# Kernel tuning notes

Hardware: AMD Instinct MI355X
Metric: run time of the kernel (lower is better)

Reference implementation:

```python
import jax, jax.numpy as jnp
import numpy as np

B, S, D_MODEL, H = 2, 2048, 2048, 16
DQK = D_MODEL // H            # 128
DV = D_MODEL * 2 // H // 3    # 85 (GLU branch)
SCALE = DQK ** -0.5
ROPE_BASE = 10000.0


def apply_rope(x):
    # x: [B, S, H, D], NeoX-style half rotation
    D = x.shape[-1]
    half = D // 2
    inv_freq = 1.0 / (ROPE_BASE ** (jnp.arange(half, dtype=jnp.float32) / half))
    ang = jnp.arange(x.shape[1], dtype=jnp.float32)[:, None] * inv_freq[None, :]  # [S, half]
    cos = jnp.cos(ang)[None, :, None, :]
    sin = jnp.sin(ang)[None, :, None, :]
    x1, x2 = x[..., :half], x[..., half:]
    return jnp.concatenate([x1 * cos - x2 * sin, x2 * cos + x1 * sin], axis=-1)


def setup_inputs() -> dict:
    key = jax.random.key(0)
    ks = jax.random.split(key, 12)
    init = lambda k, shape, fan_in: jax.random.uniform(k, shape, jnp.float32, -1.0, 1.0) * (fan_in ** -0.5)
    q = jax.random.normal(ks[0], (B, S, D_MODEL), jnp.float32)
    k = jax.random.normal(ks[1], (B, S, D_MODEL), jnp.float32)
    v = jax.random.normal(ks[2], (B, S, D_MODEL), jnp.float32)
    # causal boolean mask: True = masked (upper triangle)
    mask = jnp.triu(jnp.ones((S, S), dtype=bool), k=1)
    Wq = init(ks[3], (D_MODEL, DQK * H), D_MODEL)
    bq = init(ks[4], (DQK * H,), D_MODEL)
    Wk = init(ks[5], (D_MODEL, DQK * H), D_MODEL)
    bk = init(ks[6], (DQK * H,), D_MODEL)
    Wv = init(ks[7], (D_MODEL, DV * H * 2), D_MODEL)
    bv = init(ks[8], (DV * H * 2,), D_MODEL)
    Wo = init(ks[9], (DV * H, D_MODEL), DV * H)
    bo = init(ks[10], (D_MODEL,), DV * H)
    return {"q": q, "k": k, "v": v, "mask": mask,
            "Wq": Wq, "bq": bq, "Wk": Wk, "bk": bk,
            "Wv": Wv, "bv": bv, "Wo": Wo, "bo": bo}


def reference(q, k, v, mask, Wq, bq, Wk, bk, Wv, bv, Wo, bo):
    qp = q @ Wq + bq                      # [B,S,H*DQK]
    kp = k @ Wk + bk                      # [B,S,H*DQK]
    vp = v @ Wv + bv                      # [B,S,2*H*DV]
    # GLU over the FULL last dim (matches torch chunk(2, dim=-1) before unflatten)
    half = DV * H
    vg = vp[..., :half] * jax.nn.silu(vp[..., half:])   # [B,S,H*DV]
    qh = qp.reshape(B, S, H, DQK)
    kh = kp.reshape(B, S, H, DQK)
    vh = vg.reshape(B, S, H, DV)
    qh = apply_rope(qh)
    kh = apply_rope(kh)
    # [B,H,S,D]
    qh = qh.transpose(0, 2, 1, 3)
    kh = kh.transpose(0, 2, 1, 3)
    vh = vh.transpose(0, 2, 1, 3)
    score = jnp.einsum('bhqd,bhkd->bhqk', qh, kh) * SCALE  # [B,H,S,S]
    score = jnp.where(mask[None, None, :, :], -jnp.inf, score)
    attn = jax.nn.softmax(score, axis=-1)
    o = jnp.einsum('bhqk,bhkd->bhqd', attn, vh)            # [B,H,S,DV]
    o = o.transpose(0, 2, 1, 3).reshape(B, S, H * DV)
    return o @ Wo + bo                                     # [B,S,D_MODEL]
```

## Files before the change

kernel.cpp:

```cpp
#include <hip/hip_runtime.h>
#include <cstdint>
#include <cmath>

typedef __bf16 bf16;
typedef __bf16 bf16x8 __attribute__((ext_vector_type(8)));
typedef float f32x4 __attribute__((ext_vector_type(4)));

#define B_      2
#define S_      2048
#define H_      16
#define DQK_    128
#define DV_     85
#define DVP_    96
#define DMODEL_ 2048
#define NKV_    1360
#define KH_     1536
#define NV_     2720
#define NVP_    2816
#define SCALE_  0.08838834764831845f
#define QSCALE_ 0.12752044442215615f
#define M2_     16.0f
#define L2_10K_ 13.287712379549449f

__device__ __forceinline__ void lds_cp16(const void* g, void* l) {
    __builtin_amdgcn_global_load_lds(
        (const __attribute__((address_space(1))) unsigned int*)(uintptr_t)g,
        (__attribute__((address_space(3))) unsigned int*)(uintptr_t)l,
        16, 0, 0);
}

__global__ __launch_bounds__(256) void detect_dtype(const unsigned int* __restrict__ w,
                                                    int* __restrict__ flag) {
    __shared__ int cnt;
    if (threadIdx.x == 0) cnt = 0;
    __syncthreads();
    unsigned v = w[threadIdx.x];
    unsigned e = (v >> 7) & 0xFFu;
    if (e > 100u && e < 140u) atomicAdd(&cnt, 1);
    __syncthreads();
    if (threadIdx.x == 0) *flag = (cnt >= 200) ? 1 : 0;
}

__global__ __launch_bounds__(256) void norm_mat(const void* __restrict__ src, bf16* __restrict__ dst,
                                                const int* __restrict__ flag, long n8) {
    long i = (long)blockIdx.x * 256 + threadIdx.x;
    if (i >= n8) return;
    if (*flag) {
        ((bf16x8*)dst)[i] = ((const bf16x8*)src)[i];
    } else {
        const float* s = (const float*)src;
        bf16x8 v;
#pragma unroll
        for (int j = 0; j < 8; ++j) v[j] = (bf16)s[i * 8 + j];
        ((bf16x8*)dst)[i] = v;
    }
}

__global__ __launch_bounds__(256) void norm_bias4(
    const void* __restrict__ s0, const void* __restrict__ s1,
    const void* __restrict__ s2, const void* __restrict__ s3,
    float* __restrict__ d0, float* __restrict__ d1,
    float* __restrict__ d2, float* __restrict__ d3,
    const int* __restrict__ flag) {
    int j = blockIdx.x * 256 + threadIdx.x;
    const void* s; float* d;
    if (j < DMODEL_) { s = s0; d = d0; }
    else if ((j -= DMODEL_) < DMODEL_) { s = s1; d = d1; }
    else if ((j -= DMODEL_) < NV_) { s = s2; d = d2; }
    else if ((j -= NV_) < DMODEL_) { s = s3; d = d3; }
    else return;
    d[j] = (*flag) ? (float)((const bf16*)s)[j] : ((const float*)s)[j];
}

__global__ __launch_bounds__(256) void transpose_pad_dyn(
    const void* __restrict__ in, bf16* __restrict__ out, const int* __restrict__ flag,
    int R, int C, int Rp, int Cp) {
    __shared__ bf16 tile[32][33];
    const bool isbf = (*flag != 0);
    int r0 = blockIdx.x * 32, c0 = blockIdx.y * 32;
    int tx = threadIdx.x, ty = threadIdx.y;
#pragma unroll
    for (int i = 0; i < 32; i += 8) {
        int r = r0 + ty + i, c = c0 + tx;
        bf16 v = (bf16)0.0f;
        if (r < R && c < C) {
            size_t idx = (size_t)r * C + c;
            v = isbf ? ((const bf16*)in)[idx] : (bf16)((const float*)in)[idx];
        }
        tile[ty + i][tx] = v;
    }
    __syncthreads();
#pragma unroll
    for (int i = 0; i < 32; i += 8) {
        int oc = c0 + ty + i, orr = r0 + tx;
        if (oc < Cp && orr < Rp) out[(size_t)oc * Rp + orr] = tile[tx][ty + i];
    }
}

__global__ __launch_bounds__(256) void transpose_wo_dyn(
    const void* __restrict__ in, bf16* __restrict__ out, const int* __restrict__ flag) {
    __shared__ bf16 tile[32][33];
    const bool isbf = (*flag != 0);
    int k0 = blockIdx.x * 32, n0 = blockIdx.y * 32;
    int tx = threadIdx.x, ty = threadIdx.y;
#pragma unroll
    for (int i = 0; i < 32; i += 8) {
        int k = k0 + ty + i, c = n0 + tx;
        int hh = k / DVP_, dd = k - hh * DVP_;
        bf16 v = (bf16)0.0f;
        if (dd < DV_) {
            size_t idx = (size_t)(hh * DV_ + dd) * DMODEL_ + c;
            v = isbf ? ((const bf16*)in)[idx] : (bf16)((const float*)in)[idx];
        }
        tile[ty + i][tx] = v;
    }
    __syncthreads();
#pragma unroll
    for (int i = 0; i < 32; i += 8) {
        int n = n0 + ty + i, k = k0 + tx;
        out[(size_t)n * KH_ + k] = tile[tx][ty + i];
    }
}

__global__ __launch_bounds__(256) void gemm_qk_rope(
    const bf16* __restrict__ Aq, const bf16* __restrict__ Ak,
    const bf16* __restrict__ Btq, const bf16* __restrict__ Btk,
    const float* __restrict__ bq, const float* __restrict__ bk,
    bf16* __restrict__ qt, bf16* __restrict__ ktp) {
    __shared__ bf16 As[128 * 32];
    __shared__ bf16 Bs[128 * 32];
    __shared__ bf16 ep[64 * 132];
    const int z = blockIdx.z;
    const bf16* A    = z ? Ak  : Aq;
    const bf16* Bt   = z ? Btk : Btq;
    const float* bias = z ? bk : bq;
    bf16* dst        = z ? ktp : qt;
    const float qs   = z ? 1.0f : QSCALE_;
    const int t = threadIdx.x, lane = t & 63, w = t >> 6;
    const int m0 = blockIdx.x * 128, n0 = blockIdx.y * 128;
    const int wm = (w >> 1) * 64, wn = (w & 1) * 64;
    const int fm = lane & 15, quad = lane >> 4, fk = quad * 8;
    const int srow = lane >> 2, scol = (lane & 3) * 8;
    f32x4 acc[4][4] = {};
    for (int k0 = 0; k0 < DMODEL_; k0 += 32) {
        __syncthreads();
#pragma unroll
        for (int j = 0; j < 2; ++j) {
            int c = j * 4 + w;
            lds_cp16(A + (size_t)(m0 + c * 16 + srow) * DMODEL_ + k0 + scol, &As[c * 512]);
            lds_cp16(Bt + (size_t)(n0 + c * 16 + srow) * DMODEL_ + k0 + scol, &Bs[c * 512]);
        }
        __syncthreads();
        bf16x8 af[4], bfr[4];
#pragma unroll
        for (int i = 0; i < 4; ++i) {
            af[i]  = *(const bf16x8*)&As[(wm + i * 16 + fm) * 32 + fk];
            bfr[i] = *(const bf16x8*)&Bs[(wn + i * 16 + fm) * 32 + fk];
        }
#pragma unroll
        for (int i = 0; i < 4; ++i)
#pragma unroll
            for (int jn = 0; jn < 4; ++jn)
                acc[i][jn] = __builtin_amdgcn_mfma_f32_16x16x32_bf16(af[i], bfr[jn], acc[i][jn], 0, 0, 0);
    }
    const int h = blockIdx.y;
    const int b = m0 >> 11, s_base = m0 & (S_ - 1);
    float bv[4];
#pragma unroll
    for (int jn = 0; jn < 4; ++jn) bv[jn] = bias[n0 + wn + jn * 16 + fm];
    bf16* dbase = dst + (size_t)(b * H_ + h) * S_ * DQK_;
#pragma unroll
    for (int ph = 0; ph < 2; ++ph) {
        if ((w >> 1) == ph) {
#pragma unroll
            for (int i = 0; i < 4; ++i)
#pragma unroll
                for (int jn = 0; jn < 4; ++jn)
#pragma unroll
                    for (int r = 0; r < 4; ++r)
                        ep[(i * 16 + quad * 4 + r) * 132 + wn + jn * 16 + fm] =
                            (bf16)(acc[i][jn][r] + bv[jn]);
        }
        __syncthreads();
#pragma unroll
        for (int it2 = 0; it2 < 4; ++it2) {
            int task = it2 * 256 + t;
            int lr = task >> 4, ch = task & 15;
            int s = s_base + ph * 64 + lr;
            bf16x8 v = *(const bf16x8*)&ep[lr * 132 + ch * 8];
            bf16x8 u = *(const bf16x8*)&ep[lr * 132 + ((ch * 8) ^ 64)];
            bf16x8 o8;
#pragma unroll
            for (int j = 0; j < 8; ++j) {
                int d = ch * 8 + j, dd = d & 63;
                float ang = (float)s * exp2f(-(float)dd * (L2_10K_ / 64.0f));
                float sn, cs;
                __sincosf(ang, &sn, &cs);
                float x = (float)v[j], y = (float)u[j];
                float ov = (d < 64) ? (x * cs - y * sn) : (x * cs + y * sn);
                o8[j] = (bf16)(ov * qs);
            }
            *(bf16x8*)&dbase[(size_t)s * DQK_ + ch * 8] = o8;
        }
        __syncthreads();
    }
}

__global__ __launch_bounds__(256) void gemm_bt(
    const bf16* __restrict__ A, const bf16* __restrict__ Bt,
    const float* __restrict__ bias, bf16* __restrict__ C,
    int M, int N, int K, int Nreal, int ldc) {
    __shared__ bf16 As[128 * 32];
    __shared__ bf16 Bs[128 * 32];
    const int t = threadIdx.x, lane = t & 63, w = t >> 6;
    const int m0 = blockIdx.x * 128, n0 = blockIdx.y * 128;
    const int wm = (w >> 1) * 64, wn = (w & 1) * 64;
    const int fm = lane & 15, quad = lane >> 4, fk = quad * 8;
    const int srow = lane >> 2, scol = (lane & 3) * 8;
    f32x4 acc[4][4] = {};
    for (int k0 = 0; k0 < K; k0 += 32) {
        __syncthreads();
#pragma unroll
        for (int j = 0; j < 2; ++j) {
            int c = j * 4 + w;
            lds_cp16(A + (size_t)(m0 + c * 16 + srow) * K + k0 + scol, &As[c * 512]);
            lds_cp16(Bt + (size_t)(n0 + c * 16 + srow) * K + k0 + scol, &Bs[c * 512]);
        }
        __syncthreads();
        bf16x8 af[4], bfr[4];
#pragma unroll
        for (int i = 0; i < 4; ++i) {
            af[i]  = *(const bf16x8*)&As[(wm + i * 16 + fm) * 32 + fk];
            bfr[i] = *(const bf16x8*)&Bs[(wn + i * 16 + fm) * 32 + fk];
        }
#pragma unroll
        for (int i = 0; i < 4; ++i)
#pragma unroll
            for (int jn = 0; jn < 4; ++jn)
                acc[i][jn] = __builtin_amdgcn_mfma_f32_16x16x32_bf16(af[i], bfr[jn], acc[i][jn], 0, 0, 0);
    }
#pragma unroll
    for (int jn = 0; jn < 4; ++jn) {
        int col = n0 + wn + jn * 16 + fm;
        if (col >= Nreal) continue;
        float bv = bias[col];
#pragma unroll
        for (int i = 0; i < 4; ++i) {
            int rowb = m0 + wm + i * 16 + quad * 4;
#pragma unroll
            for (int r = 0; r < 4; ++r)
                C[(size_t)(rowb + r) * ldc + col] = (bf16)(acc[i][jn][r] + bv);
        }
    }
}

__global__ __launch_bounds__(256) void gemm_bt_oh(
    const bf16* __restrict__ Oh, const bf16* __restrict__ Bt,
    const float* __restrict__ bias, bf16* __restrict__ C, float* __restrict__ Cf,
    const int* __restrict__ outflag) {
    __shared__ bf16 As[128 * 32];
    __shared__ bf16 Bs[128 * 32];
    const int t = threadIdx.x, lane = t & 63, w = t >> 6;
    const int m0 = blockIdx.x * 128, n0 = blockIdx.y * 128;
    const int wm = (w >> 1) * 64, wn = (w & 1) * 64;
    const int fm = lane & 15, quad = lane >> 4, fk = quad * 8;
    const int srow = lane >> 2, scol = (lane & 3) * 8;
    f32x4 acc[4][4] = {};
    for (int k0 = 0; k0 < KH_; k0 += 32) {
        __syncthreads();
#pragma unroll
        for (int j = 0; j < 2; ++j) {
            int c = j * 4 + w;
            int m = m0 + c * 16 + srow;
            int k = k0 + scol;
            int hh = k / DVP_, dd = k - hh * DVP_;
            const bf16* ga = Oh + ((size_t)((m >> 11) * H_ + hh) * S_ + (m & (S_ - 1))) * DVP_ + dd;
            lds_cp16(ga, &As[c * 512]);
            lds_cp16(Bt + (size_t)(n0 + c * 16 + srow) * KH_ + k0 + scol, &Bs[c * 512]);
        }
        __syncthreads();
        bf16x8 af[4], bfr[4];
#pragma unroll
        for (int i = 0; i < 4; ++i) {
            af[i]  = *(const bf16x8*)&As[(wm + i * 16 + fm) * 32 + fk];
            bfr[i] = *(const bf16x8*)&Bs[(wn + i * 16 + fm) * 32 + fk];
        }
#pragma unroll
        for (int i = 0; i < 4; ++i)
#pragma unroll
            for (int jn = 0; jn < 4; ++jn)
                acc[i][jn] = __builtin_amdgcn_mfma_f32_16x16x32_bf16(af[i], bfr[jn], acc[i][jn], 0, 0, 0);
    }
    bool bf16out = (*outflag != 0);
#pragma unroll
    for (int jn = 0; jn < 4; ++jn) {
        int col = n0 + wn + jn * 16 + fm;
        float bv = bias[col];
#pragma unroll
        for (int i = 0; i < 4; ++i) {
            int rowb = m0 + wm + i * 16 + quad * 4;
            if (bf16out) {
#pragma unroll
                for (int r = 0; r < 4; ++r)
                    C[(size_t)(rowb + r) * DMODEL_ + col] = (bf16)(acc[i][jn][r] + bv);
            } else {
#pragma unroll
                for (int r = 0; r < 4; ++r)
                    Cf[(size_t)(rowb + r) * DMODEL_ + col] = acc[i][jn][r] + bv;
            }
        }
    }
}

__global__ __launch_bounds__(256) void swiglu_tr2(const bf16* __restrict__ vp, bf16* __restrict__ vt) {
    __shared__ bf16 tile[32][33];
    const int bh = blockIdx.x, b = bh >> 4, h = bh & 15;
    const int s0 = blockIdx.y * 32, d0 = blockIdx.z * 32;
    const int tx = threadIdx.x, ty = threadIdx.y;
#pragma unroll
    for (int i = 0; i < 32; i += 8) {
        int s = s0 + ty + i, d = d0 + tx;
        float val = 0.0f;
        if (d < DV_) {
            size_t row = (size_t)(b * S_ + s) * NV_ + h * DV_ + d;
            float a = (float)vp[row];
            float g = (float)vp[row + NKV_];
            val = a * g / (1.0f + __expf(-g));
        } else if (d == 95) {
            val = 1.0f;
        }
        tile[ty + i][tx] = (bf16)val;
    }
    __syncthreads();
#pragma unroll
    for (int i = 0; i < 32; i += 8) {
        int d = d0 + ty + i, s = s0 + tx;
        vt[((size_t)bh * DVP_ + d) * S_ + s] = tile[tx][ty + i];
    }
}

__global__ __launch_bounds__(256) void attn_split(
    const bf16* __restrict__ qt, const bf16* __restrict__ kt,
    const bf16* __restrict__ vt,
    bf16* __restrict__ Opart, float* __restrict__ lpart) {
    const int bh = blockIdx.x, qb = blockIdx.y, split = blockIdx.z;
    if (split * 8 > qb) return;
    __shared__ bf16 Ks[64 * 128];
    __shared__ bf16 Vs[96 * 64];
    __shared__ bf16 plds[4][16 * 72];
    const int t = threadIdx.x, lane = t & 63, w = t >> 6;
    const int fm = lane & 15, quad = lane >> 4;
    const int h = bh & 15, b = bh >> 4;
    const int q0 = qb * 64 + w * 16;
    const int g = qb >> 3;
    const int pidx = bh * 80 + 4 * g * (g + 1) + (qb & 7) * (g + 1) + split;

    const bf16* qbase = qt + ((size_t)(b * H_ + h) * S_ + q0 + fm) * DQK_ + quad * 8;
    bf16x8 aq[4];
#pragma unroll
    for (int kb = 0; kb < 4; ++kb) aq[kb] = *(const bf16x8*)(qbase + kb * 32);
    const bf16* kbase = kt + (size_t)(b * H_ + h) * S_ * DQK_;
    const bf16* vbase = vt + (size_t)(b * H_ + h) * DVP_ * S_;

    const float NEG_INF = -__builtin_inff();
    f32x4 oacc[6] = {};
    bf16* pl = &plds[w][0];

    const int t0 = split * 8;
    const int t1 = min(t0 + 8, qb + 1);
    for (int it = t0; it < t1; ++it) {
        const int k0 = it * 64;
        __syncthreads();
#pragma unroll
        for (int iw = 0; iw < 4; ++iw) {
            int flat = (w * 4 + iw) * 64 + lane;
            int r = flat >> 4, c = (flat & 15) ^ (r & 15);
            lds_cp16(kbase + (size_t)(k0 + r) * DQK_ + c * 8, &Ks[(w * 4 + iw) * 512]);
        }
#pragma unroll
        for (int iw = 0; iw < 3; ++iw) {
            int flat = (w * 3 + iw) * 64 + lane;
            int r = flat >> 3, c = (flat & 7) ^ (r & 7);
            lds_cp16(vbase + (size_t)r * S_ + k0 + c * 8, &Vs[(w * 3 + iw) * 512]);
        }
        __syncthreads();
        f32x4 sc[4] = {};
#pragma unroll
        for (int nt = 0; nt < 4; ++nt) {
            if (k0 + nt * 16 <= q0 + 15) {
                const int row16 = (nt * 16 + fm) * 16;
#pragma unroll
                for (int kb = 0; kb < 4; ++kb) {
                    const bf16* kp = &Ks[(row16 + ((kb * 4 + quad) ^ fm)) * 8];
                    sc[nt] = __builtin_amdgcn_mfma_f32_16x16x32_bf16(aq[kb], *(const bf16x8*)kp, sc[nt], 0, 0, 0);
                }
            }
        }
        if (it == qb) {
#pragma unroll
            for (int nt = 0; nt < 4; ++nt) {
                int col = k0 + nt * 16 + fm;
#pragma unroll
                for (int r = 0; r < 4; ++r) {
                    int rowq = q0 + quad * 4 + r;
                    if (col > rowq) sc[nt][r] = NEG_INF;
                }
            }
        }
#pragma unroll
        for (int nt = 0; nt < 4; ++nt)
#pragma unroll
            for (int r = 0; r < 4; ++r)
                pl[(quad * 4 + r) * 72 + nt * 16 + fm] =
                    (bf16)__builtin_amdgcn_exp2f(sc[nt][r] - M2_);
        asm volatile("s_waitcnt lgkmcnt(0)" ::: "memory");
        bf16x8 pa0 = *(const bf16x8*)(pl + fm * 72 + quad * 8);
        bf16x8 pa1 = *(const bf16x8*)(pl + fm * 72 + 32 + quad * 8);
#pragma unroll
        for (int n2 = 0; n2 < 6; ++n2) {
            int row8 = (n2 * 16 + fm) * 8;
            const bf16* v0 = &Vs[(row8 + (quad ^ (fm & 7))) * 8];
            const bf16* v1 = &Vs[(row8 + ((4 + quad) ^ (fm & 7))) * 8];
            oacc[n2] = __builtin_amdgcn_mfma_f32_16x16x32_bf16(pa0, *(const bf16x8*)v0, oacc[n2], 0, 0, 0);
            oacc[n2] = __builtin_amdgcn_mfma_f32_16x16x32_bf16(pa1, *(const bf16x8*)v1, oacc[n2], 0, 0, 0);
        }
    }
    float lv[4], inv_l[4];
#pragma unroll
    for (int r = 0; r < 4; ++r) {
        lv[r] = __shfl(oacc[5][r], (lane & 48) | 15, 64);
        inv_l[r] = (lv[r] > 0.f) ? 1.0f / lv[r] : 0.0f;
    }
    if (fm == 0) {
#pragma unroll
        for (int r = 0; r < 4; ++r) {
            int row = w * 16 + quad * 4 + r;
            lpart[(size_t)pidx * 64 + row] = lv[r];
        }
    }
#pragma unroll
    for (int n2 = 0; n2 < 6; ++n2)
#pragma unroll
        for (int r = 0; r < 4; ++r) {
            int row = w * 16 + quad * 4 + r;
            Opart[((size_t)pidx * 64 + row) * DVP_ + n2 * 16 + fm] = (bf16)(oacc[n2][r] * inv_l[r]);
        }
}

__global__ __launch_bounds__(256) void attn_combine2(
    const bf16* __restrict__ Opart, const float* __restrict__ lpart,
    bf16* __restrict__ oh) {
    const int bh = blockIdx.x, qb = blockIdx.y;
    const int g = qb >> 3, nact = g + 1;
    const int pidx0 = bh * 80 + 4 * g * (g + 1) + (qb & 7) * (g + 1);
    const int t = threadIdx.x;
#pragma unroll
    for (int i = 0; i < 3; ++i) {
        int idx = i * 256 + t;
        int row = idx / 12, ch = idx - row * 12;
        float W = 0.f, wgt[4];
        for (int p = 0; p < nact; ++p) {
            wgt[p] = lpart[(size_t)(pidx0 + p) * 64 + row];
            W += wgt[p];
        }
        float invW = (W > 0.f) ? 1.0f / W : 0.0f;
        float acc[8] = {};
        for (int p = 0; p < nact; ++p) {
            bf16x8 v = *(const bf16x8*)&Opart[((size_t)(pidx0 + p) * 64 + row) * DVP_ + ch * 8];
#pragma unroll
            for (int j = 0; j < 8; ++j) acc[j] += wgt[p] * (float)v[j];
        }
        bf16x8 o8;
#pragma unroll
        for (int j = 0; j < 8; ++j) o8[j] = (bf16)(acc[j] * invW);
        *(bf16x8*)&oh[((size_t)bh * S_ + qb * 64 + row) * DVP_ + ch * 8] = o8;
    }
}

extern "C" void kernel_launch(void* const* d_in, const int* in_sizes, int n_in,
                              void* d_out, int out_size, void* d_ws, size_t ws_size,
                              hipStream_t stream) {
    const void* qin = d_in[0];
    const void* kin = d_in[1];
    const void* vin = d_in[2];
    const void* Wq = d_in[4];
    const void* bq = d_in[5];
    const void* Wk = d_in[6];
    const void* bk = d_in[7];
    const void* Wv = d_in[8];
    const void* bv = d_in[9];
    const void* Wo = d_in[10];
    const void* bo = d_in[11];

    char* ws = (char*)d_ws;
    bf16* qt   = (bf16*)(ws);
    bf16* ktp  = (bf16*)(ws + 16777216);
    char* R1   = ws + 33554432;
    bf16* scrq = (bf16*)(R1);
    bf16* scrk = (bf16*)(R1 + 16777216);
    bf16* wTq  = (bf16*)(R1 + 33554432);
    bf16* wTk  = (bf16*)(R1 + 41943040);
    bf16* scrv  = (bf16*)(R1);
    bf16* wTv   = (bf16*)(R1 + 16777216);
    bf16* projv = (bf16*)(R1 + 28311552);
    bf16*  wTo   = (bf16*)(R1);
    bf16*  Opart = (bf16*)(R1 + 6291456);
    float* lpart = (float*)(R1 + 37748736);
    bf16* vtp = (bf16*)(ws + 84148224);
    bf16* oh  = (bf16*)(ws + 96731136);
    float* bqf = (float*)(ws + 109314048);
    float* bkf = bqf + DMODEL_;
    float* bvf = bkf + DMODEL_;
    float* bof = bvf + NV_;
    int*  flag = (int*)(bof + DMODEL_);

    dim3 tb(32, 8);
    auto nblk = [](long n8) { return (int)((n8 + 255) / 256); };
    long n8_x = (long)B_ * S_ * DMODEL_ / 8;

    detect_dtype<<<1, 256, 0, stream>>>((const unsigned int*)qin, flag);
    norm_bias4<<<(3 * DMODEL_ + NV_ + 255) / 256, 256, 0, stream>>>(
        bq, bk, bv, bo, bqf, bkf, bvf, bof, flag);

    norm_mat<<<nblk(n8_x), 256, 0, stream>>>(qin, scrq, flag, n8_x);
    norm_mat<<<nblk(n8_x), 256, 0, stream>>>(kin, scrk, flag, n8_x);
    transpose_pad_dyn<<<dim3(64, 64), tb, 0, stream>>>(Wq, wTq, flag, DMODEL_, DMODEL_, DMODEL_, DMODEL_);
    transpose_pad_dyn<<<dim3(64, 64), tb, 0, stream>>>(Wk, wTk, flag, DMODEL_, DMODEL_, DMODEL_, DMODEL_);
    gemm_qk_rope<<<dim3(32, 16, 2), 256, 0, stream>>>(scrq, scrk, wTq, wTk, bqf, bkf, qt, ktp);

    norm_mat<<<nblk(n8_x), 256, 0, stream>>>(vin, scrv, flag, n8_x);
    transpose_pad_dyn<<<dim3(64, NVP_ / 32), tb, 0, stream>>>(Wv, wTv, flag, DMODEL_, NV_, DMODEL_, NVP_);
    gemm_bt<<<dim3(32, NVP_ / 128), 256, 0, stream>>>(scrv, wTv, bvf, projv, 4096, NVP_, 2048, NV_, NV_);
    swiglu_tr2<<<dim3(B_ * H_, S_ / 32, 3), tb, 0, stream>>>(projv, vtp);

    transpose_wo_dyn<<<dim3(KH_ / 32, DMODEL_ / 32), tb, 0, stream>>>(Wo, wTo, flag);

    attn_split<<<dim3(32, 32, 4), 256, 0, stream>>>(qt, ktp, vtp, Opart, lpart);
    attn_combine2<<<dim3(32, 32), 256, 0, stream>>>(Opart, lpart, oh);

    gemm_bt_oh<<<dim3(32, 16), 256, 0, stream>>>(oh, wTo, bof, (bf16*)d_out, (float*)d_out, flag);
}
```

Before: 528.9 us.

## Fuse SwiGLU and V transpose into V-projection GEMM epilogue via interleaved Wv

The Wv transpose now interleaves value and gate columns so that each value/gate pair lands in adjacent lanes of the GEMM output. The V GEMM epilogue then applies SwiGLU through a lane shuffle, stages the result in LDS and writes the head-transposed vt layout directly. This removes the projv intermediate round trip and the separate swiglu_tr2 kernel. A small vt_pad kernel fills the padding rows, and the Wq/Wk transposes are merged into a single launch.

```diff
diff --git a/kernel.cpp b/kernel.cpp
--- a/kernel.cpp
+++ b/kernel.cpp
@@ -72,29 +72,48 @@
     d[j] = (*flag) ? (float)((const bf16*)s)[j] : ((const float*)s)[j];
 }
 
-__global__ __launch_bounds__(256) void transpose_pad_dyn(
-    const void* __restrict__ in, bf16* __restrict__ out, const int* __restrict__ flag,
-    int R, int C, int Rp, int Cp) {
+__global__ __launch_bounds__(256) void transpose_qk_dyn(
+    const void* __restrict__ inq, const void* __restrict__ ink,
+    bf16* __restrict__ outq, bf16* __restrict__ outk, const int* __restrict__ flag) {
     __shared__ bf16 tile[32][33];
     const bool isbf = (*flag != 0);
+    const void* in = blockIdx.z ? ink : inq;
+    bf16* out = blockIdx.z ? outk : outq;
     int r0 = blockIdx.x * 32, c0 = blockIdx.y * 32;
     int tx = threadIdx.x, ty = threadIdx.y;
 #pragma unroll
     for (int i = 0; i < 32; i += 8) {
-        int r = r0 + ty + i, c = c0 + tx;
+        size_t idx = (size_t)(r0 + ty + i) * DMODEL_ + c0 + tx;
+        tile[ty + i][tx] = isbf ? ((const bf16*)in)[idx] : (bf16)((const float*)in)[idx];
+    }
+    __syncthreads();
+#pragma unroll
+    for (int i = 0; i < 32; i += 8)
+        out[(size_t)(c0 + ty + i) * DMODEL_ + r0 + tx] = tile[tx][ty + i];
+}
+
+__global__ __launch_bounds__(256) void transpose_wvi_dyn(
+    const void* __restrict__ in, bf16* __restrict__ out, const int* __restrict__ flag) {
+    __shared__ bf16 tile[32][34];
+    const bool isbf = (*flag != 0);
+    int n0 = blockIdx.x * 32, k0 = blockIdx.y * 32;
+    int tx = threadIdx.x, ty = threadIdx.y;
+    int fl = (n0 >> 1) + (tx & 15), vg = tx >> 4;
+    int c = vg * NKV_ + fl;
+    int nl = 2 * (tx & 15) + vg;
+#pragma unroll
+    for (int i = 0; i < 32; i += 8) {
         bf16 v = (bf16)0.0f;
-        if (r < R && c < C) {
-            size_t idx = (size_t)r * C + c;
+        if (fl < NKV_) {
+            size_t idx = (size_t)(k0 + ty + i) * NV_ + c;
             v = isbf ? ((const bf16*)in)[idx] : (bf16)((const float*)in)[idx];
         }
-        tile[ty + i][tx] = v;
+        tile[ty + i][nl] = v;
     }
     __syncthreads();
 #pragma unroll
-    for (int i = 0; i < 32; i += 8) {
-        int oc = c0 + ty + i, orr = r0 + tx;
-        if (oc < Cp && orr < Rp) out[(size_t)oc * Rp + orr] = tile[tx][ty + i];
-    }
+    for (int i = 0; i < 32; i += 8)
+        out[(size_t)(n0 + ty + i) * DMODEL_ + k0 + tx] = tile[tx][ty + i];
 }
 
 __global__ __launch_bounds__(256) void transpose_wo_dyn(
@@ -206,25 +225,25 @@
     }
 }
 
-__global__ __launch_bounds__(256) void gemm_bt(
+__global__ __launch_bounds__(256) void gemm_v_swiglu(
     const bf16* __restrict__ A, const bf16* __restrict__ Bt,
-    const float* __restrict__ bias, bf16* __restrict__ C,
-    int M, int N, int K, int Nreal, int ldc) {
+    const float* __restrict__ bias, bf16* __restrict__ vt) {
     __shared__ bf16 As[128 * 32];
     __shared__ bf16 Bs[128 * 32];
+    __shared__ bf16 ep2[64 * 136];
     const int t = threadIdx.x, lane = t & 63, w = t >> 6;
     const int m0 = blockIdx.x * 128, n0 = blockIdx.y * 128;
     const int wm = (w >> 1) * 64, wn = (w & 1) * 64;
     const int fm = lane & 15, quad = lane >> 4, fk = quad * 8;
     const int srow = lane >> 2, scol = (lane & 3) * 8;
     f32x4 acc[4][4] = {};
-    for (int k0 = 0; k0 < K; k0 += 32) {
+    for (int k0 = 0; k0 < DMODEL_; k0 += 32) {
         __syncthreads();
 #pragma unroll
         for (int j = 0; j < 2; ++j) {
             int c = j * 4 + w;
-            lds_cp16(A + (size_t)(m0 + c * 16 + srow) * K + k0 + scol, &As[c * 512]);
-            lds_cp16(Bt + (size_t)(n0 + c * 16 + srow) * K + k0 + scol, &Bs[c * 512]);
+            lds_cp16(A + (size_t)(m0 + c * 16 + srow) * DMODEL_ + k0 + scol, &As[c * 512]);
+            lds_cp16(Bt + (size_t)(n0 + c * 16 + srow) * DMODEL_ + k0 + scol, &Bs[c * 512]);
         }
         __syncthreads();
         bf16x8 af[4], bfr[4];
@@ -239,19 +258,53 @@
             for (int jn = 0; jn < 4; ++jn)
                 acc[i][jn] = __builtin_amdgcn_mfma_f32_16x16x32_bf16(af[i], bfr[jn], acc[i][jn], 0, 0, 0);
     }
+    float bv[4];
 #pragma unroll
     for (int jn = 0; jn < 4; ++jn) {
         int col = n0 + wn + jn * 16 + fm;
-        if (col >= Nreal) continue;
-        float bv = bias[col];
-#pragma unroll
-        for (int i = 0; i < 4; ++i) {
-            int rowb = m0 + wm + i * 16 + quad * 4;
-#pragma unroll
-            for (int r = 0; r < 4; ++r)
-                C[(size_t)(rowb + r) * ldc + col] = (bf16)(acc[i][jn][r] + bv);
-        }
-    }
+        bv[jn] = (col < NV_) ? bias[(col & 1) * NKV_ + (col >> 1)] : 0.0f;
+    }
+    const bool isval = ((fm & 1) == 0);
+    const int fl_base = (wn >> 1) + (fm >> 1);
+    const int s_base = wm + quad * 4;
+#pragma unroll
+    for (int i = 0; i < 4; ++i)
+#pragma unroll
+        for (int jn = 0; jn < 4; ++jn)
+#pragma unroll
+            for (int r = 0; r < 4; ++r) {
+                float ag = acc[i][jn][r] + bv[jn];
+                float part = __shfl_xor(ag, 1, 64);
+                if (isval) {
+                    float g = part;
+                    float out = ag * g / (1.0f + __expf(-g));
+                    ep2[(fl_base + jn * 8) * 136 + s_base + i * 16 + r] = (bf16)out;
+                }
+            }
+    __syncthreads();
+    const int b = m0 >> 11, s0 = m0 & (S_ - 1);
+#pragma unroll
+    for (int it2 = 0; it2 < 4; ++it2) {
+        int task = it2 * 256 + t;
+        int fl_local = task >> 4, ch = task & 15;
+        int flat = blockIdx.y * 64 + fl_local;
+        if (flat < NKV_) {
+            int h = (flat * 1543) >> 17;
+            int d = flat - h * DV_;
+            bf16x8 v = *(const bf16x8*)&ep2[fl_local * 136 + ch * 8];
+            *(bf16x8*)&vt[((size_t)(b * H_ + h) * DVP_ + d) * S_ + s0 + ch * 8] = v;
+        }
+    }
+}
+
+__global__ __launch_bounds__(256) void vt_pad(bf16* __restrict__ vt) {
+    int idx = blockIdx.x * 256 + threadIdx.x;
+    if (idx >= 32 * 11 * 2048) return;
+    int s = idx & (S_ - 1);
+    int rest = idx >> 11;
+    int dpad = 85 + rest % 11;
+    int bh = rest / 11;
+    vt[((size_t)bh * DVP_ + dpad) * S_ + s] = (bf16)((dpad == 95) ? 1.0f : 0.0f);
 }
 
 __global__ __launch_bounds__(256) void gemm_bt_oh(
@@ -309,33 +362,6 @@
                     Cf[(size_t)(rowb + r) * DMODEL_ + col] = acc[i][jn][r] + bv;
             }
         }
-    }
-}
-
-__global__ __launch_bounds__(256) void swiglu_tr2(const bf16* __restrict__ vp, bf16* __restrict__ vt) {
-    __shared__ bf16 tile[32][33];
-    const int bh = blockIdx.x, b = bh >> 4, h = bh & 15;
-    const int s0 = blockIdx.y * 32, d0 = blockIdx.z * 32;
-    const int tx = threadIdx.x, ty = threadIdx.y;
-#pragma unroll
-    for (int i = 0; i < 32; i += 8) {
-        int s = s0 + ty + i, d = d0 + tx;
-        float val = 0.0f;
-        if (d < DV_) {
-            size_t row = (size_t)(b * S_ + s) * NV_ + h * DV_ + d;
-            float a = (float)vp[row];
-            float g = (float)vp[row + NKV_];
-            val = a * g / (1.0f + __expf(-g));
-        } else if (d == 95) {
-            val = 1.0f;
-        }
-        tile[ty + i][tx] = (bf16)val;
-    }
-    __syncthreads();
-#pragma unroll
-    for (int i = 0; i < 32; i += 8) {
-        int d = d0 + ty + i, s = s0 + tx;
-        vt[((size_t)bh * DVP_ + d) * S_ + s] = tile[tx][ty + i];
     }
 }
 
@@ -500,9 +526,8 @@
     bf16* scrk = (bf16*)(R1 + 16777216);
     bf16* wTq  = (bf16*)(R1 + 33554432);
     bf16* wTk  = (bf16*)(R1 + 41943040);
-    bf16* scrv  = (bf16*)(R1);
-    bf16* wTv   = (bf16*)(R1 + 16777216);
-    bf16* projv = (bf16*)(R1 + 28311552);
+    bf16* scrv = (bf16*)(R1);
+    bf16* wTvi = (bf16*)(R1 + 16777216);
     bf16*  wTo   = (bf16*)(R1);
     bf16*  Opart = (bf16*)(R1 + 6291456);
     float* lpart = (float*)(R1 + 37748736);
@@ -521,17 +546,16 @@
     detect_dtype<<<1, 256, 0, stream>>>((const unsigned int*)qin, flag);
     norm_bias4<<<(3 * DMODEL_ + NV_ + 255) / 256, 256, 0, stream>>>(
         bq, bk, bv, bo, bqf, bkf, bvf, bof, flag);
+    vt_pad<<<(32 * 11 * 2048) / 256, 256, 0, stream>>>(vtp);
 
     norm_mat<<<nblk(n8_x), 256, 0, stream>>>(qin, scrq, flag, n8_x);
     norm_mat<<<nblk(n8_x), 256, 0, stream>>>(kin, scrk, flag, n8_x);
-    transpose_pad_dyn<<<dim3(64, 64), tb, 0, stream>>>(Wq, wTq, flag, DMODEL_, DMODEL_, DMODEL_, DMODEL_);
-    transpose_pad_dyn<<<dim3(64, 64), tb, 0, stream>>>(Wk, wTk, flag, DMODEL_, DMODEL_, DMODEL_, DMODEL_);
+    transpose_qk_dyn<<<dim3(64, 64, 2), tb, 0, stream>>>(Wq, Wk, wTq, wTk, flag);
     gemm_qk_rope<<<dim3(32, 16, 2), 256, 0, stream>>>(scrq, scrk, wTq, wTk, bqf, bkf, qt, ktp);
 
     norm_mat<<<nblk(n8_x), 256, 0, stream>>>(vin, scrv, flag, n8_x);
-    transpose_pad_dyn<<<dim3(64, NVP_ / 32), tb, 0, stream>>>(Wv, wTv, flag, DMODEL_, NV_, DMODEL_, NVP_);
-    gemm_bt<<<dim3(32, NVP_ / 128), 256, 0, stream>>>(scrv, wTv, bvf, projv, 4096, NVP_, 2048, NV_, NV_);
-    swiglu_tr2<<<dim3(B_ * H_, S_ / 32, 3), tb, 0, stream>>>(projv, vtp);
+    transpose_wvi_dyn<<<dim3(NVP_ / 32, DMODEL_ / 32), tb, 0, stream>>>(Wv, wTvi, flag);
+    gemm_v_swiglu<<<dim3(32, NVP_ / 128), 256, 0, stream>>>(scrv, wTvi, bvf, vtp);
 
     transpose_wo_dyn<<<dim3(KH_ / 32, DMODEL_ / 32), tb, 0, stream>>>(Wo, wTo, flag);
 
```

Measured after the change: 509.4 us. -3.7%, faster.
